# Kernel optimization log

Hardware: AMD Instinct MI355X
Metric: run time of the kernel (lower is better)

## Reference

```python
import jax, jax.numpy as jnp
import numpy as np

N_PTS, N_NODES, N_CMP = 2048, 8192, 1024
CHUNK = 4  # cmp columns per scan step; bounds the [P, CHUNK, N] intermediate


def setup_inputs() -> dict:
    key = jax.random.key(0)
    k1, k2 = jax.random.split(key)
    x = jax.random.normal(k1, (N_PTS, N_NODES), dtype=jnp.float32)
    # learned edge states; EDG_NULL == 0, so mask = (states != 0)
    learned_edge_states = jax.random.randint(k2, (N_NODES, N_CMP), 0, 2, dtype=jnp.int32)
    return {"x": x, "learned_edge_states": learned_edge_states}


def _masked_colmax(x, mask):
    """x: [P, N] float; mask: [N, C] bool -> [P, C] max of x over masked nodes per column.

    Columns with no nonzero entries yield 0.0 (original leaves the zero-initialized output).
    Chunked over C to avoid materializing the full [P, N, C] tensor.
    """
    neg_inf = jnp.float32(-jnp.inf)
    P = x.shape[0]
    C = mask.shape[1]
    mask_chunks = mask.T.reshape(C // CHUNK, CHUNK, -1)  # [S, CHUNK, N]

    def step(carry, m):
        # m: [CHUNK, N]; masked max over node axis -> [P, CHUNK]
        vals = jnp.max(jnp.where(m[None, :, :], x[:, None, :], neg_inf), axis=2)
        return carry, vals

    _, out = jax.lax.scan(step, None, mask_chunks)  # [S, P, CHUNK]
    out = jnp.transpose(out, (1, 0, 2)).reshape(P, C)
    has_any = jnp.any(mask, axis=0)  # [C]
    return jnp.where(has_any[None, :], out, jnp.float32(0.0))


def reference(x, learned_edge_states):
    mask = learned_edge_states != 0
    return _masked_colmax(x, mask)
```

## Files before the change

### kernel.cpp

```cpp
#include <hip/hip_runtime.h>
#include <hip/hip_bf16.h>
#include <math.h>

#define N_PTS   2048
#define N_NODES 8192
#define N_CMP   1024
#define CAP     128
#define K_MIN   32
#define K_MAX   112
#define TOPK    64
#define THR     2.5f


__device__ __forceinline__ unsigned int float_to_key(float f) {
    unsigned int b = __float_as_uint(f);
    return (b & 0x80000000u) ? ~b : (b | 0x80000000u);
}

__global__ __launch_bounds__(256) void pack_kernel(const int* __restrict__ states,
                                                   unsigned int* __restrict__ bitsT) {
    int t    = threadIdx.x;
    int lane = t & 63;
    int W    = blockIdx.x * 4 + (t >> 6);
    int n    = W >> 4;
    int cg   = W & 15;
    int s    = states[(size_t)n * N_CMP + cg * 64 + lane];
    unsigned long long m = __ballot(s != 0);
    if (lane == 0) {
        bitsT[n * 32 + cg * 2]     = (unsigned int)(m & 0xffffffffull);
        bitsT[n * 32 + cg * 2 + 1] = (unsigned int)(m >> 32);
    }
}

__global__ __launch_bounds__(256, 8) void row_kernel(const float* __restrict__ x,
                                                     const unsigned int* __restrict__ bitsT,
                                                     float* __restrict__ out) {
    const int p    = blockIdx.x;
    const int t    = threadIdx.x;
    const int lane = t & 63;
    const int wv   = t >> 6;

    __shared__ float        s_val[CAP];
    __shared__ int          s_id[CAP];
    __shared__ float        s_sval[TOPK];
    __shared__ int          s_sid[TOPK];
    __shared__ unsigned int s_cnt[4];
    __shared__ unsigned int s_mask[4][16][2];
    __shared__ int          s_num;
    __shared__ int          s_flag;

    if (t == 0) { s_num = 0; s_flag = 0; }
    __syncthreads();

    const float4* row4 = reinterpret_cast<const float4*>(x + (size_t)p * N_NODES);

#define CAND_TEST(F, IDX) do { float _f = (F); \
    if (_f >= THR) { int _pos = atomicAdd(&s_num, 1); \
        if (_pos < CAP) { s_val[_pos] = _f; s_id[_pos] = (IDX); } } } while (0)

#pragma unroll
    for (int j = 0; j < 8; j++) {
        float4 v  = row4[j * 256 + t];
        int bidx  = (j * 256 + t) * 4;
        CAND_TEST(v.x, bidx);
        CAND_TEST(v.y, bidx + 1);
        CAND_TEST(v.z, bidx + 2);
        CAND_TEST(v.w, bidx + 3);
    }
    __syncthreads();
    int L = s_num;

    if (L < K_MIN || L > CAP) {
        unsigned int lo = 0u, hi = 0xFFFFFFFFu;
        unsigned int Tk = float_to_key(THR);
        if (L > CAP) lo = Tk; else hi = Tk;
        for (int it = 0; it < 34 && (hi - lo) > 1u; ++it) {
            unsigned int mid = lo + ((hi - lo) >> 1);
            int myc = 0;
#pragma unroll
            for (int j = 0; j < 8; j++) {
                float4 v = row4[j * 256 + t];
                myc += (int)__popcll(__ballot(float_to_key(v.x) >= mid));
                myc += (int)__popcll(__ballot(float_to_key(v.y) >= mid));
                myc += (int)__popcll(__ballot(float_to_key(v.z) >= mid));
                myc += (int)__popcll(__ballot(float_to_key(v.w) >= mid));
            }
            if (lane == 0) s_cnt[wv] = (unsigned int)myc;
            __syncthreads();
            int c = (int)(s_cnt[0] + s_cnt[1] + s_cnt[2] + s_cnt[3]);
            __syncthreads();
            if (c >= K_MIN) { lo = mid; if (c <= K_MAX) break; }
            else            hi = mid;
        }
        if (t == 0) s_num = 0;
        __syncthreads();
#pragma unroll
        for (int j = 0; j < 8; j++) {
            float4 v = row4[j * 256 + t];
            int bidx = (j * 256 + t) * 4;
#define CAND_TEST2(F, IDX) do { float _f = (F); \
    if (float_to_key(_f) >= lo) { int _pos = atomicAdd(&s_num, 1); \
        if (_pos < CAP) { s_val[_pos] = _f; s_id[_pos] = (IDX); } } } while (0)
            CAND_TEST2(v.x, bidx);
            CAND_TEST2(v.y, bidx + 1);
            CAND_TEST2(v.z, bidx + 2);
            CAND_TEST2(v.w, bidx + 3);
#undef CAND_TEST2
        }
        __syncthreads();
        L = s_num;
        if (t == 0 && (L > CAP || L < 1)) s_flag = 1;
        if (L > CAP) L = CAP;
        __syncthreads();
    }
#undef CAND_TEST

    int flag = s_flag;

    if (!flag && t < L) {
        float mv = s_val[t];
        int   mi = s_id[t];
        int r = 0;
        for (int j = 0; j < L; ++j) {
            float vj = s_val[j];
            r += (int)((vj > mv) | ((vj == mv) & (j < t)));
        }
        if (r < TOPK) { s_sval[r] = mv; s_sid[r] = mi; }
    }
    __syncthreads();

    int Lc = (L < TOPK) ? L : TOPK;

    for (int i = 0; i < 4; ++i) {
        int cg = wv * 4 + i;
        int c  = cg * 64 + lane;
        int fidx = -1;

        if (!flag) {
            for (int k0 = 0; k0 < Lc; k0 += 16) {
                int j16 = lane & 15;
                int kk  = k0 + j16;
                unsigned int m0 = 0, m1 = 0;
                if (lane < 16 && kk < Lc) {
                    const unsigned int* bp = bitsT + (size_t)s_sid[kk] * 32 + cg * 2;
                    m0 = bp[0];
                    m1 = bp[1];
                }
                if (lane < 16) { s_mask[wv][j16][0] = m0; s_mask[wv][j16][1] = m1; }
                __asm__ volatile("s_waitcnt lgkmcnt(0)" ::: "memory");
                unsigned int hits = 0;
                int half = lane >> 5;
                int bit  = lane & 31;
#pragma unroll
                for (int k = 0; k < 16; k++) {
                    hits |= ((s_mask[wv][k][half] >> bit) & 1u) << k;
                }
                if (fidx < 0 && hits) fidx = k0 + (int)__builtin_ctz(hits);
                if (__all(fidx >= 0)) break;
            }
        }

        float res;
        if (fidx >= 0) {
            res = s_sval[fidx];
        } else {
            const float* row = x + (size_t)p * N_NODES;
            float mm = -INFINITY;
            for (int n = 0; n < N_NODES; n++) {
                unsigned int w = bitsT[n * 32 + (c >> 5)];
                if ((w >> (c & 31)) & 1u) mm = fmaxf(mm, row[n]);
            }
            res = (mm == -INFINITY) ? 0.0f : mm;
        }
        out[(size_t)p * N_CMP + c] = res;
    }
}

extern "C" void kernel_launch(void* const* d_in, const int* in_sizes, int n_in,
                              void* d_out, int out_size, void* d_ws, size_t ws_size,
                              hipStream_t stream) {
    const float* x      = (const float*)d_in[0];
    const int*   states = (const int*)d_in[1];
    float*       out    = (float*)d_out;
    unsigned int* bitsT = (unsigned int*)d_ws;

    pack_kernel<<<(N_NODES * (N_CMP / 64)) / 4, 256, 0, stream>>>(states, bitsT);
    row_kernel<<<N_PTS, 256, 0, stream>>>(x, bitsT, out);
}
```

Baseline: 147.8 us.

## Drop bit-packing pre-pass and read edge states directly for top candidates

New measurement: 129.6 us. 12.3% less time.

```diff
diff --git a/kernel.cpp b/kernel.cpp
--- a/kernel.cpp
+++ b/kernel.cpp
@@ -5,156 +5,106 @@
 #define N_PTS   2048
 #define N_NODES 8192
 #define N_CMP   1024
-#define CAP     128
+#define CAP     256
 #define K_MIN   32
-#define K_MAX   112
+#define K_ACC   16
 #define TOPK    64
-#define THR     2.5f
+#define THR1    2.5f
+#define THR2    2.0f
 
 
-__device__ __forceinline__ unsigned int float_to_key(float f) {
-    unsigned int b = __float_as_uint(f);
-    return (b & 0x80000000u) ? ~b : (b | 0x80000000u);
-}
-
-__global__ __launch_bounds__(256) void pack_kernel(const int* __restrict__ states,
-                                                   unsigned int* __restrict__ bitsT) {
-    int t    = threadIdx.x;
-    int lane = t & 63;
-    int W    = blockIdx.x * 4 + (t >> 6);
-    int n    = W >> 4;
-    int cg   = W & 15;
-    int s    = states[(size_t)n * N_CMP + cg * 64 + lane];
-    unsigned long long m = __ballot(s != 0);
-    if (lane == 0) {
-        bitsT[n * 32 + cg * 2]     = (unsigned int)(m & 0xffffffffull);
-        bitsT[n * 32 + cg * 2 + 1] = (unsigned int)(m >> 32);
-    }
-}
-
-__global__ __launch_bounds__(256, 8) void row_kernel(const float* __restrict__ x,
-                                                     const unsigned int* __restrict__ bitsT,
-                                                     float* __restrict__ out) {
+__global__ __launch_bounds__(256, 4) void hnet_kernel(const float* __restrict__ x,
+                                                      const int* __restrict__ states,
+                                                      float* __restrict__ out) {
     const int p    = blockIdx.x;
     const int t    = threadIdx.x;
     const int lane = t & 63;
     const int wv   = t >> 6;
 
-    __shared__ float        s_val[CAP];
-    __shared__ int          s_id[CAP];
-    __shared__ float        s_sval[TOPK];
-    __shared__ int          s_sid[TOPK];
-    __shared__ unsigned int s_cnt[4];
-    __shared__ unsigned int s_mask[4][16][2];
-    __shared__ int          s_num;
-    __shared__ int          s_flag;
+    __shared__ float s_val[CAP];
+    __shared__ int   s_id[CAP];
+    __shared__ float s_sval[TOPK];
+    __shared__ int   s_sid[TOPK];
+    __shared__ int   s_num;
+    __shared__ char  s_pad[33 * 1024];
 
-    if (t == 0) { s_num = 0; s_flag = 0; }
+    if (t == 0) s_num = 0;
+    if ((int)blockIdx.y == 1) s_pad[t] = 0;
     __syncthreads();
 
     const float4* row4 = reinterpret_cast<const float4*>(x + (size_t)p * N_NODES);
 
-#define CAND_TEST(F, IDX) do { float _f = (F); \
-    if (_f >= THR) { int _pos = atomicAdd(&s_num, 1); \
-        if (_pos < CAP) { s_val[_pos] = _f; s_id[_pos] = (IDX); } } } while (0)
+    float4 r[8];
+#pragma unroll
+    for (int j = 0; j < 8; j++) r[j] = row4[j * 256 + t];
 
+#define PUSH(F, IDX) do { float _f = (F); int _q = atomicAdd(&s_num, 1); \
+    if (_q < CAP) { s_val[_q] = _f; s_id[_q] = (IDX); } } while (0)
 #pragma unroll
     for (int j = 0; j < 8; j++) {
-        float4 v  = row4[j * 256 + t];
-        int bidx  = (j * 256 + t) * 4;
-        CAND_TEST(v.x, bidx);
-        CAND_TEST(v.y, bidx + 1);
-        CAND_TEST(v.z, bidx + 2);
-        CAND_TEST(v.w, bidx + 3);
+        float4 v = r[j];
+        int bidx = (j * 256 + t) * 4;
+        if (v.x >= THR1) PUSH(v.x, bidx);
+        if (v.y >= THR1) PUSH(v.y, bidx + 1);
+        if (v.z >= THR1) PUSH(v.z, bidx + 2);
+        if (v.w >= THR1) PUSH(v.w, bidx + 3);
     }
     __syncthreads();
     int L = s_num;
 
-    if (L < K_MIN || L > CAP) {
-        unsigned int lo = 0u, hi = 0xFFFFFFFFu;
-        unsigned int Tk = float_to_key(THR);
-        if (L > CAP) lo = Tk; else hi = Tk;
-        for (int it = 0; it < 34 && (hi - lo) > 1u; ++it) {
-            unsigned int mid = lo + ((hi - lo) >> 1);
-            int myc = 0;
-#pragma unroll
-            for (int j = 0; j < 8; j++) {
-                float4 v = row4[j * 256 + t];
-                myc += (int)__popcll(__ballot(float_to_key(v.x) >= mid));
-                myc += (int)__popcll(__ballot(float_to_key(v.y) >= mid));
-                myc += (int)__popcll(__ballot(float_to_key(v.z) >= mid));
-                myc += (int)__popcll(__ballot(float_to_key(v.w) >= mid));
-            }
-            if (lane == 0) s_cnt[wv] = (unsigned int)myc;
-            __syncthreads();
-            int c = (int)(s_cnt[0] + s_cnt[1] + s_cnt[2] + s_cnt[3]);
-            __syncthreads();
-            if (c >= K_MIN) { lo = mid; if (c <= K_MAX) break; }
-            else            hi = mid;
-        }
-        if (t == 0) s_num = 0;
-        __syncthreads();
+    if (L < K_MIN) {
 #pragma unroll
         for (int j = 0; j < 8; j++) {
-            float4 v = row4[j * 256 + t];
+            float4 v = r[j];
             int bidx = (j * 256 + t) * 4;
-#define CAND_TEST2(F, IDX) do { float _f = (F); \
-    if (float_to_key(_f) >= lo) { int _pos = atomicAdd(&s_num, 1); \
-        if (_pos < CAP) { s_val[_pos] = _f; s_id[_pos] = (IDX); } } } while (0)
-            CAND_TEST2(v.x, bidx);
-            CAND_TEST2(v.y, bidx + 1);
-            CAND_TEST2(v.z, bidx + 2);
-            CAND_TEST2(v.w, bidx + 3);
-#undef CAND_TEST2
+            if (v.x >= THR2 && v.x < THR1) PUSH(v.x, bidx);
+            if (v.y >= THR2 && v.y < THR1) PUSH(v.y, bidx + 1);
+            if (v.z >= THR2 && v.z < THR1) PUSH(v.z, bidx + 2);
+            if (v.w >= THR2 && v.w < THR1) PUSH(v.w, bidx + 3);
         }
         __syncthreads();
         L = s_num;
-        if (t == 0 && (L > CAP || L < 1)) s_flag = 1;
-        if (L > CAP) L = CAP;
-        __syncthreads();
     }
-#undef CAND_TEST
+#undef PUSH
 
-    int flag = s_flag;
+    const int flag = (L > CAP) | (L < K_ACC);
 
     if (!flag && t < L) {
         float mv = s_val[t];
         int   mi = s_id[t];
-        int r = 0;
+        int rk = 0;
         for (int j = 0; j < L; ++j) {
             float vj = s_val[j];
-            r += (int)((vj > mv) | ((vj == mv) & (j < t)));
+            rk += (int)((vj > mv) | ((vj == mv) & (j < t)));
         }
-        if (r < TOPK) { s_sval[r] = mv; s_sid[r] = mi; }
+        if (rk < TOPK) { s_sval[rk] = mv; s_sid[rk] = mi; }
     }
     __syncthreads();
+    const int Lc = (L < TOPK) ? L : TOPK;
 
-    int Lc = (L < TOPK) ? L : TOPK;
-
+#pragma unroll 1
     for (int i = 0; i < 4; ++i) {
         int cg = wv * 4 + i;
         int c  = cg * 64 + lane;
         int fidx = -1;
 
         if (!flag) {
+#pragma unroll 1
             for (int k0 = 0; k0 < Lc; k0 += 16) {
-                int j16 = lane & 15;
-                int kk  = k0 + j16;
-                unsigned int m0 = 0, m1 = 0;
-                if (lane < 16 && kk < Lc) {
-                    const unsigned int* bp = bitsT + (size_t)s_sid[kk] * 32 + cg * 2;
-                    m0 = bp[0];
-                    m1 = bp[1];
+                int kmax = Lc - k0;
+                if (kmax > 16) kmax = 16;
+                int sv[16];
+#pragma unroll
+                for (int j = 0; j < 16; j++) {
+                    if (j < kmax) {
+                        int n = __builtin_amdgcn_readfirstlane(s_sid[k0 + j]);
+                        sv[j] = states[(size_t)n * N_CMP + c];
+                    }
                 }
-                if (lane < 16) { s_mask[wv][j16][0] = m0; s_mask[wv][j16][1] = m1; }
-                __asm__ volatile("s_waitcnt lgkmcnt(0)" ::: "memory");
                 unsigned int hits = 0;
-                int half = lane >> 5;
-                int bit  = lane & 31;
 #pragma unroll
-                for (int k = 0; k < 16; k++) {
-                    hits |= ((s_mask[wv][k][half] >> bit) & 1u) << k;
-                }
+                for (int j = 0; j < 16; j++)
+                    if (j < kmax && sv[j] != 0) hits |= (1u << j);
                 if (fidx < 0 && hits) fidx = k0 + (int)__builtin_ctz(hits);
                 if (__all(fidx >= 0)) break;
             }
@@ -167,8 +117,7 @@
             const float* row = x + (size_t)p * N_NODES;
             float mm = -INFINITY;
             for (int n = 0; n < N_NODES; n++) {
-                unsigned int w = bitsT[n * 32 + (c >> 5)];
-                if ((w >> (c & 31)) & 1u) mm = fmaxf(mm, row[n]);
+                if (states[(size_t)n * N_CMP + c] != 0) mm = fmaxf(mm, row[n]);
             }
             res = (mm == -INFINITY) ? 0.0f : mm;
         }
@@ -182,8 +131,6 @@
     const float* x      = (const float*)d_in[0];
     const int*   states = (const int*)d_in[1];
     float*       out    = (float*)d_out;
-    unsigned int* bitsT = (unsigned int*)d_ws;
 
-    pack_kernel<<<(N_NODES * (N_CMP / 64)) / 4, 256, 0, stream>>>(states, bitsT);
-    row_kernel<<<N_PTS, 256, 0, stream>>>(x, bitsT, out);
+    hnet_kernel<<<N_PTS, 256, 0, stream>>>(x, states, out);
 }
```
